# Performance work log

Hardware: AMD Instinct MI355X
Metric: run time of the kernel (lower is better)

## Reference

```python
import jax, jax.numpy as jnp
import numpy as np

TAU = 0.5
EPS = 1e-08
NORM_EPS = 1e-12  # F.normalize clamp

BS = 4096
D = 256


def _l2_normalize(x):
    n = jnp.linalg.norm(x, axis=1, keepdims=True)
    return x / jnp.maximum(n, NORM_EPS)


def setup_inputs() -> dict:
    key = jax.random.key(0)
    k1, k2 = jax.random.split(key)
    zi = jax.random.normal(k1, (BS, D), dtype=jnp.float32)
    zj = jax.random.normal(k2, (BS, D), dtype=jnp.float32)
    return {"zi": zi, "zj": zj}


def reference(zi, zj):
    bs = zi.shape[0]
    zi_n = _l2_normalize(zi)
    zj_n = _l2_normalize(zj)
    z = jnp.concatenate([zi_n, zj_n], axis=0)  # [2bs, d]
    # cosine sim of unit vectors == dot product
    sim = (z @ z.T) / TAU  # [2bs, 2bs]
    # positive pairs: (i, i+bs) and (i+bs, i) -> same diag values twice
    pos_diag = jnp.sum(zi_n * zj_n, axis=1) / TAU  # [bs]
    sim_pos = jnp.exp(jnp.concatenate([pos_diag, pos_diag]))  # [2bs]
    # negatives: all off-diagonal entries per row
    exp_sim = jnp.exp(sim)
    neg_sum = jnp.sum(exp_sim, axis=1) - jnp.diagonal(exp_sim)  # [2bs]
    loss = jnp.mean(-jnp.log(sim_pos / (neg_sum + EPS)))
    return loss
```

## Files before the change

kernel.cpp:

```cpp
#include <hip/hip_runtime.h>

#define N_TOT 8192
#define BSZ   4096
#define DIM   256

typedef __attribute__((ext_vector_type(4))) float f32x4;
typedef __attribute__((ext_vector_type(2))) unsigned long long u64x2;

#define PRESCALE 1.69864362f

__device__ __forceinline__ void async_copy16(const void* g, void* l) {
    __builtin_amdgcn_global_load_lds((const __attribute__((address_space(1))) void*)g,
                                     (__attribute__((address_space(3))) void*)l,
                                     16, 0, 0);
}

__global__ __launch_bounds__(256) void norm_kernel(const float* __restrict__ zi,
                                                   const float* __restrict__ zj,
                                                   unsigned char* __restrict__ zb,
                                                   float* __restrict__ posPart) {
    __shared__ float buf[2][256];
    const int wid  = threadIdx.x >> 6;
    const int lane = threadIdx.x & 63;
    const int pair = blockIdx.x * 2 + (wid & 1);
    const bool isZj = (wid >= 2);
    const float* src = isZj ? (zj + (size_t)pair * DIM) : (zi + (size_t)pair * DIM);
    float4 v = ((const float4*)src)[lane];
    float ss = v.x * v.x + v.y * v.y + v.z * v.z + v.w * v.w;
    #pragma unroll
    for (int off = 1; off < 64; off <<= 1) ss += __shfl_xor(ss, off);
    float inv = 1.0f / fmaxf(sqrtf(ss), 1e-12f);
    float4 nv = make_float4(v.x * inv, v.y * inv, v.z * inv, v.w * inv);

    const int outRow = isZj ? (pair + BSZ) : pair;
    const int j8  = lane >> 1;
    const int off4 = ((j8 >> 3) << 6) + ((j8 & 3) << 4) + (((j8 >> 2) & 1) << 3)
                   + ((lane & 1) << 2);
    int pk = __builtin_amdgcn_cvt_pk_fp8_f32(nv.x * PRESCALE, nv.y * PRESCALE, 0, false);
    pk     = __builtin_amdgcn_cvt_pk_fp8_f32(nv.z * PRESCALE, nv.w * PRESCALE, pk, true);
    *(int*)(zb + (size_t)outRow * 256 + off4) = pk;

    if (!isZj) ((float4*)&buf[wid & 1][0])[lane] = nv;
    __syncthreads();
    if (isZj) {
        float4 a = ((float4*)&buf[wid & 1][0])[lane];
        float d = a.x * nv.x + a.y * nv.y + a.z * nv.z + a.w * nv.w;
        #pragma unroll
        for (int off = 1; off < 64; off <<= 1) d += __shfl_xor(d, off);
        if (lane == 0) posPart[pair] = d;
    }
}

__global__ __launch_bounds__(256, 4) void sim_kernel(const unsigned char* __restrict__ zb,
                                                     float* __restrict__ partial) {
    __shared__ alignas(16) char smem[32768];

    const int t    = threadIdx.x;
    const int lane = t & 63;
    const int wid  = t >> 6;
    const int wr   = wid >> 1;
    const int wc   = wid & 1;
    const int g    = lane >> 4;
    const int c15  = lane & 15;

    const int k = blockIdx.x;
    int bi = (int)((129.0f - sqrtf(16641.0f - 8.0f * (float)k)) * 0.5f);
    while (bi * 64 - bi * (bi - 1) / 2 > k) bi--;
    while ((bi + 1) * 64 - (bi + 1) * bi / 2 <= k) bi++;
    const int bj = bi + (k - (bi * 64 - bi * (bi - 1) / 2));
    const bool diag = (bi == bj);

    const int row0 = bi * 128;
    const int col0 = bj * 128;

    f32x4 acc[4][4];
    #pragma unroll
    for (int m = 0; m < 4; m++)
        #pragma unroll
        for (int n = 0; n < 4; n++) acc[m][n] = (f32x4){0.f, 0.f, 0.f, 0.f};

    #define STAGE(b, kt) do {                                                   \
        _Pragma("unroll")                                                       \
        for (int i = 0; i < 2; i++) {                                           \
            const int e_  = i * 256 + t;                   \
            const int rr_ = e_ >> 2;                       \
            const int p_  = e_ & 3;                             \
            const int g_  = p_ ^ ((rr_ >> 1) & 3);           \
            char* lb = smem + (b) * 16384 + (i * 256 + wid * 64) * 16;          \
            async_copy16(zb + (size_t)(row0 + rr_) * 256 + (kt) * 64 + g_ * 16, \
                         lb);                                                   \
            async_copy16(zb + (size_t)(col0 + rr_) * 256 + (kt) * 64 + g_ * 16, \
                         lb + 8192);                                            \
        } } while (0)

    STAGE(0, 0);

    #pragma unroll
    for (int kt = 0; kt < 4; ++kt) {
        const int cur = kt & 1;
        if (kt < 3) {
            STAGE(cur ^ 1, kt + 1);
            asm volatile("s_waitcnt vmcnt(4)" ::: "memory");
        } else {
            asm volatile("s_waitcnt vmcnt(0)" ::: "memory");
        }
        __builtin_amdgcn_sched_barrier(0);
        __builtin_amdgcn_s_barrier();

        const char* Ab = smem + cur * 16384;
        const char* Bb = Ab + 8192;
        u64x2 af[4], bfr[4];
        #pragma unroll
        for (int m = 0; m < 4; m++) {
            const int rr = wr * 64 + m * 16 + c15;
            const int p  = g ^ ((rr >> 1) & 3);
            af[m] = *(const u64x2*)(Ab + rr * 64 + p * 16);
        }
        #pragma unroll
        for (int n = 0; n < 4; n++) {
            const int rr = wc * 64 + n * 16 + c15;
            const int p  = g ^ ((rr >> 1) & 3);
            bfr[n] = *(const u64x2*)(Bb + rr * 64 + p * 16);
        }
        #pragma unroll
        for (int m = 0; m < 4; m++)
            #pragma unroll
            for (int n = 0; n < 4; n++) {
                acc[m][n] = __builtin_amdgcn_mfma_f32_16x16x32_fp8_fp8(
                    (long)af[m].x, (long)bfr[n].x, acc[m][n], 0, 0, 0);
                acc[m][n] = __builtin_amdgcn_mfma_f32_16x16x32_fp8_fp8(
                    (long)af[m].y, (long)bfr[n].y, acc[m][n], 0, 0, 0);
            }

        __builtin_amdgcn_sched_barrier(0);
        __builtin_amdgcn_s_barrier();
    }
    #undef STAGE

    float rsum[4][4];
    float csum[4];
    #pragma unroll
    for (int m = 0; m < 4; m++)
        #pragma unroll
        for (int j = 0; j < 4; j++) rsum[m][j] = 0.f;
    #pragma unroll
    for (int n = 0; n < 4; n++) csum[n] = 0.f;

    const int colbase = col0 + wc * 64 + c15;
    const int rowbase = row0 + wr * 64 + (g << 2);
    #pragma unroll
    for (int m = 0; m < 4; m++) {
        #pragma unroll
        for (int n = 0; n < 4; n++) {
            const int colg = colbase + n * 16;
            #pragma unroll
            for (int j = 0; j < 4; j++) {
                const int rowg = rowbase + m * 16 + j;
                float e = exp2f(acc[m][n][j]);
                if (diag && rowg == colg) e = 0.0f;
                rsum[m][j] += e;
                csum[n] += e;
            }
        }
    }

    if (!diag) {
        #pragma unroll
        for (int n = 0; n < 4; n++) {
            float s = csum[n];
            s += __shfl_xor(s, 16);
            s += __shfl_xor(s, 32);
            csum[n] = s;
        }
        if (lane < 16) {
            float* dst = partial + (size_t)(bi * 2 + wr) * N_TOT;
            #pragma unroll
            for (int n = 0; n < 4; n++)
                dst[colbase + n * 16] = csum[n];
        }
    }

    float* sw = (float*)smem + wid * 1280;
    #pragma unroll
    for (int m = 0; m < 4; m++)
        #pragma unroll
        for (int j = 0; j < 4; j++)
            sw[(m * 16 + (g << 2) + j) * 20 + c15] = rsum[m][j];
    asm volatile("s_waitcnt lgkmcnt(0)" ::: "memory");
    __builtin_amdgcn_sched_barrier(0);
    f32x4 v0 = *(const f32x4*)(sw + lane * 20 + 0);
    f32x4 v1 = *(const f32x4*)(sw + lane * 20 + 4);
    f32x4 v2 = *(const f32x4*)(sw + lane * 20 + 8);
    f32x4 v3 = *(const f32x4*)(sw + lane * 20 + 12);
    float tot = (v0[0] + v0[1] + v0[2] + v0[3]) + (v1[0] + v1[1] + v1[2] + v1[3])
              + (v2[0] + v2[1] + v2[2] + v2[3]) + (v3[0] + v3[1] + v3[2] + v3[3]);
    partial[(size_t)(bj * 2 + wc) * N_TOT + row0 + wr * 64 + lane] = tot;
}

__global__ __launch_bounds__(256) void rowlog_kernel(const float* __restrict__ partial,
                                                     float* __restrict__ logPart) {
    const int lane = threadIdx.x & 63;
    const int w    = threadIdx.x >> 6;
    const int row  = blockIdx.x * 64 + lane;
    float s = 0.f;
    #pragma unroll 8
    for (int p = w * 32; p < w * 32 + 32; p++) s += partial[(size_t)p * N_TOT + row];
    __shared__ float red[4][64];
    red[w][lane] = s;
    __syncthreads();
    if (w == 0) {
        float tot = red[0][lane] + red[1][lane] + red[2][lane] + red[3][lane];
        float v = logf(tot + 1e-8f);
        #pragma unroll
        for (int off = 1; off < 64; off <<= 1) v += __shfl_xor(v, off);
        if (lane == 0) logPart[blockIdx.x] = v;
    }
}

__global__ __launch_bounds__(256) void final_kernel(const float* __restrict__ logPart,
                                                    const float* __restrict__ posPart,
                                                    float* __restrict__ out) {
    const int t = threadIdx.x;
    float ps = 0.f;
    for (int i = t; i < BSZ; i += 256) ps += posPart[i];
    float ls = (t < 128) ? logPart[t] : 0.f;
    #pragma unroll
    for (int off = 1; off < 64; off <<= 1) {
        ps += __shfl_xor(ps, off);
        ls += __shfl_xor(ls, off);
    }
    __shared__ float redp[4], redl[4];
    const int lane = t & 63, wid = t >> 6;
    if (lane == 0) { redp[wid] = ps; redl[wid] = ls; }
    __syncthreads();
    if (t == 0) {
        const float posSum = redp[0] + redp[1] + redp[2] + redp[3];
        const float logSum = redl[0] + redl[1] + redl[2] + redl[3];
        out[0] = logSum / (float)N_TOT - 2.0f * posSum / (float)BSZ;
    }
}

extern "C" void kernel_launch(void* const* d_in, const int* in_sizes, int n_in,
                              void* d_out, int out_size, void* d_ws, size_t ws_size,
                              hipStream_t stream) {
    const float* zi = (const float*)d_in[0];
    const float* zj = (const float*)d_in[1];
    float* out = (float*)d_out;

    char* ws = (char*)d_ws;
    unsigned char* zb = (unsigned char*)ws;
    float* partial     = (float*)(ws + (size_t)(4 << 20));
    float* logPart     = (float*)(ws + (size_t)(8 << 20));
    float* posPart     = (float*)(ws + (size_t)(8 << 20) + 4096);

    norm_kernel<<<2048, 256, 0, stream>>>(zi, zj, zb, posPart);
    sim_kernel<<<2080, 256, 0, stream>>>(zb, partial);
    rowlog_kernel<<<128, 256, 0, stream>>>(partial, logPart);
    final_kernel<<<1, 256, 0, stream>>>(logPart, posPart, out);
}
```

Before: 38.57 us.

## Switch sim GEMM to scaled 16x16x128 FP8 MFMA with two-stage full-K loads

Replaces the pairs of 16x16x32 fp8 MFMAs with the gfx950 scaled 16x16x128 f8f6f4 MFMA (unit scales), which cuts the instruction count per K-step. The fp8 row layout is changed to plain linear order and the LDS swizzle is redone for 128-byte K chunks. Both K halves are loaded into a doubled 64KB LDS buffer up front, replacing the 4-step double-buffered loop. Occupancy hint drops from 4 to 2 blocks per CU, which reduces latency hiding across blocks.

```diff
diff --git a/kernel.cpp b/kernel.cpp
--- a/kernel.cpp
+++ b/kernel.cpp
@@ -5,9 +5,11 @@
 #define DIM   256
 
 typedef __attribute__((ext_vector_type(4))) float f32x4;
-typedef __attribute__((ext_vector_type(2))) unsigned long long u64x2;
+typedef __attribute__((ext_vector_type(4))) int   i32x4;
+typedef __attribute__((ext_vector_type(8))) int   i32x8;
 
 #define PRESCALE 1.69864362f
+#define SCALE1   0x7F7F7F7F
 
 __device__ __forceinline__ void async_copy16(const void* g, void* l) {
     __builtin_amdgcn_global_load_lds((const __attribute__((address_space(1))) void*)g,
@@ -33,12 +35,9 @@
     float4 nv = make_float4(v.x * inv, v.y * inv, v.z * inv, v.w * inv);
 
     const int outRow = isZj ? (pair + BSZ) : pair;
-    const int j8  = lane >> 1;
-    const int off4 = ((j8 >> 3) << 6) + ((j8 & 3) << 4) + (((j8 >> 2) & 1) << 3)
-                   + ((lane & 1) << 2);
     int pk = __builtin_amdgcn_cvt_pk_fp8_f32(nv.x * PRESCALE, nv.y * PRESCALE, 0, false);
     pk     = __builtin_amdgcn_cvt_pk_fp8_f32(nv.z * PRESCALE, nv.w * PRESCALE, pk, true);
-    *(int*)(zb + (size_t)outRow * 256 + off4) = pk;
+    *(int*)(zb + (size_t)outRow * 256 + lane * 4) = pk;
 
     if (!isZj) ((float4*)&buf[wid & 1][0])[lane] = nv;
     __syncthreads();
@@ -51,9 +50,9 @@
     }
 }
 
-__global__ __launch_bounds__(256, 4) void sim_kernel(const unsigned char* __restrict__ zb,
+__global__ __launch_bounds__(256, 2) void sim_kernel(const unsigned char* __restrict__ zb,
                                                      float* __restrict__ partial) {
-    __shared__ alignas(16) char smem[32768];
+    __shared__ alignas(16) char smem[65536];
 
     const int t    = threadIdx.x;
     const int lane = t & 63;
@@ -79,63 +78,63 @@
         #pragma unroll
         for (int n = 0; n < 4; n++) acc[m][n] = (f32x4){0.f, 0.f, 0.f, 0.f};
 
-    #define STAGE(b, kt) do {                                                   \
+    #define STAGE(kt) do {                                                      \
         _Pragma("unroll")                                                       \
-        for (int i = 0; i < 2; i++) {                                           \
-            const int e_  = i * 256 + t;                   \
-            const int rr_ = e_ >> 2;                       \
-            const int p_  = e_ & 3;                             \
-            const int g_  = p_ ^ ((rr_ >> 1) & 3);           \
-            char* lb = smem + (b) * 16384 + (i * 256 + wid * 64) * 16;          \
-            async_copy16(zb + (size_t)(row0 + rr_) * 256 + (kt) * 64 + g_ * 16, \
-                         lb);                                                   \
-            async_copy16(zb + (size_t)(col0 + rr_) * 256 + (kt) * 64 + g_ * 16, \
-                         lb + 8192);                                            \
+        for (int i = 0; i < 4; i++) {                                           \
+            const int e_  = i * 256 + t;                  \
+            const int rr_ = e_ >> 3;                       \
+            const int c_  = (e_ & 7) ^ (((rr_ >> 2) & 1) << 1);                 \
+            char* lb = smem + (kt) * 32768 + (i * 256 + wid * 64) * 16;         \
+            const size_t ko = (size_t)(kt) * 128 + c_ * 16;                     \
+            async_copy16(zb + (size_t)(row0 + rr_) * 256 + ko, lb);             \
+            async_copy16(zb + (size_t)(col0 + rr_) * 256 + ko, lb + 16384);     \
         } } while (0)
 
-    STAGE(0, 0);
-
-    #pragma unroll
-    for (int kt = 0; kt < 4; ++kt) {
-        const int cur = kt & 1;
-        if (kt < 3) {
-            STAGE(cur ^ 1, kt + 1);
-            asm volatile("s_waitcnt vmcnt(4)" ::: "memory");
-        } else {
-            asm volatile("s_waitcnt vmcnt(0)" ::: "memory");
-        }
-        __builtin_amdgcn_sched_barrier(0);
-        __builtin_amdgcn_s_barrier();
-
-        const char* Ab = smem + cur * 16384;
-        const char* Bb = Ab + 8192;
-        u64x2 af[4], bfr[4];
+    STAGE(0);
+    STAGE(1);
+    asm volatile("s_waitcnt vmcnt(8)" ::: "memory");
+    __builtin_amdgcn_sched_barrier(0);
+    __builtin_amdgcn_s_barrier();
+
+    #pragma unroll
+    for (int kt = 0; kt < 2; ++kt) {
+        const char* Ab = smem + kt * 32768;
+        const char* Bb = Ab + 16384;
+        i32x8 af[4], bfr[4];
         #pragma unroll
         for (int m = 0; m < 4; m++) {
             const int rr = wr * 64 + m * 16 + c15;
-            const int p  = g ^ ((rr >> 1) & 3);
-            af[m] = *(const u64x2*)(Ab + rr * 64 + p * 16);
+            const int pp = g ^ ((rr >> 2) & 1);
+            i32x4 lo = *(const i32x4*)(Ab + rr * 128 + pp * 32);
+            i32x4 hi = *(const i32x4*)(Ab + rr * 128 + pp * 32 + 16);
+            af[m] = __builtin_shufflevector(lo, hi, 0, 1, 2, 3, 4, 5, 6, 7);
         }
         #pragma unroll
         for (int n = 0; n < 4; n++) {
             const int rr = wc * 64 + n * 16 + c15;
-            const int p  = g ^ ((rr >> 1) & 3);
-            bfr[n] = *(const u64x2*)(Bb + rr * 64 + p * 16);
+            const int pp = g ^ ((rr >> 2) & 1);
+            i32x4 lo = *(const i32x4*)(Bb + rr * 128 + pp * 32);
+            i32x4 hi = *(const i32x4*)(Bb + rr * 128 + pp * 32 + 16);
+            bfr[n] = __builtin_shufflevector(lo, hi, 0, 1, 2, 3, 4, 5, 6, 7);
         }
         #pragma unroll
         for (int m = 0; m < 4; m++)
             #pragma unroll
-            for (int n = 0; n < 4; n++) {
-                acc[m][n] = __builtin_amdgcn_mfma_f32_16x16x32_fp8_fp8(
-                    (long)af[m].x, (long)bfr[n].x, acc[m][n], 0, 0, 0);
-                acc[m][n] = __builtin_amdgcn_mfma_f32_16x16x32_fp8_fp8(
-                    (long)af[m].y, (long)bfr[n].y, acc[m][n], 0, 0, 0);
-            }
-
-        __builtin_amdgcn_sched_barrier(0);
-        __builtin_amdgcn_s_barrier();
+            for (int n = 0; n < 4; n++)
+                acc[m][n] = __builtin_amdgcn_mfma_scale_f32_16x16x128_f8f6f4(
+                    af[m], bfr[n], acc[m][n], 0, 0, 0, SCALE1, 0, SCALE1);
+
+        if (kt == 0) {
+            asm volatile("s_waitcnt vmcnt(0)" ::: "memory");
+            __builtin_amdgcn_sched_barrier(0);
+            __builtin_amdgcn_s_barrier();
+        }
     }
     #undef STAGE
+
+    asm volatile("s_waitcnt lgkmcnt(0)" ::: "memory");
+    __builtin_amdgcn_sched_barrier(0);
+    __builtin_amdgcn_s_barrier();
 
     float rsum[4][4];
     float csum[4];
```

Measured after the change: 41.41 us. +7.4%, slower.

## Switch similarity GEMM to 32x32x64 scaled FP8 MFMA with new LDS layout

Applied to the files above, without the earlier changes.

Replaces the 16x16x32 FP8 MFMA tiles with the 32x32x64 f8f6f4 scaled MFMA (unit scales), so each wave issues 4 large MFMAs per k-step instead of 32 small ones. The FP8 row layout in global memory is made contiguous, the LDS swizzle is changed to match the new fragment loads, and the epilogue row/column reductions are rewritten for the 32x32 accumulator layout with a swizzled LDS transpose. This cuts instruction issue and fragment-load overhead at the cost of a more complex epilogue and larger per-lane fragments.

```diff
diff --git a/kernel.cpp b/kernel.cpp
--- a/kernel.cpp
+++ b/kernel.cpp
@@ -4,10 +4,13 @@
 #define BSZ   4096
 #define DIM   256
 
-typedef __attribute__((ext_vector_type(4))) float f32x4;
-typedef __attribute__((ext_vector_type(2))) unsigned long long u64x2;
+typedef __attribute__((ext_vector_type(4)))  float f32x4;
+typedef __attribute__((ext_vector_type(16))) float f32x16;
+typedef __attribute__((ext_vector_type(4)))  int   i32x4;
+typedef __attribute__((ext_vector_type(8)))  int   i32x8;
 
 #define PRESCALE 1.69864362f
+#define SCALE1   0x7F7F7F7F
 
 __device__ __forceinline__ void async_copy16(const void* g, void* l) {
     __builtin_amdgcn_global_load_lds((const __attribute__((address_space(1))) void*)g,
@@ -33,12 +36,9 @@
     float4 nv = make_float4(v.x * inv, v.y * inv, v.z * inv, v.w * inv);
 
     const int outRow = isZj ? (pair + BSZ) : pair;
-    const int j8  = lane >> 1;
-    const int off4 = ((j8 >> 3) << 6) + ((j8 & 3) << 4) + (((j8 >> 2) & 1) << 3)
-                   + ((lane & 1) << 2);
     int pk = __builtin_amdgcn_cvt_pk_fp8_f32(nv.x * PRESCALE, nv.y * PRESCALE, 0, false);
     pk     = __builtin_amdgcn_cvt_pk_fp8_f32(nv.z * PRESCALE, nv.w * PRESCALE, pk, true);
-    *(int*)(zb + (size_t)outRow * 256 + off4) = pk;
+    *(int*)(zb + (size_t)outRow * 256 + lane * 4) = pk;
 
     if (!isZj) ((float4*)&buf[wid & 1][0])[lane] = nv;
     __syncthreads();
@@ -60,8 +60,8 @@
     const int wid  = t >> 6;
     const int wr   = wid >> 1;
     const int wc   = wid & 1;
-    const int g    = lane >> 4;
-    const int c15  = lane & 15;
+    const int hi   = lane >> 5;
+    const int r31  = lane & 31;
 
     const int k = blockIdx.x;
     int bi = (int)((129.0f - sqrtf(16641.0f - 8.0f * (float)k)) * 0.5f);
@@ -73,11 +73,13 @@
     const int row0 = bi * 128;
     const int col0 = bj * 128;
 
-    f32x4 acc[4][4];
-    #pragma unroll
-    for (int m = 0; m < 4; m++)
-        #pragma unroll
-        for (int n = 0; n < 4; n++) acc[m][n] = (f32x4){0.f, 0.f, 0.f, 0.f};
+    f32x16 acc[2][2];
+    #pragma unroll
+    for (int mt = 0; mt < 2; mt++)
+        #pragma unroll
+        for (int nt = 0; nt < 2; nt++)
+            #pragma unroll
+            for (int r = 0; r < 16; r++) acc[mt][nt][r] = 0.f;
 
     #define STAGE(b, kt) do {                                                   \
         _Pragma("unroll")                                                       \
@@ -85,7 +87,7 @@
             const int e_  = i * 256 + t;                   \
             const int rr_ = e_ >> 2;                       \
             const int p_  = e_ & 3;                             \
-            const int g_  = p_ ^ ((rr_ >> 1) & 3);           \
+            const int g_  = p_ ^ ((rr_ >> 2) & 3);           \
             char* lb = smem + (b) * 16384 + (i * 256 + wid * 64) * 16;          \
             async_copy16(zb + (size_t)(row0 + rr_) * 256 + (kt) * 64 + g_ * 16, \
                          lb);                                                   \
@@ -109,91 +111,72 @@
 
         const char* Ab = smem + cur * 16384;
         const char* Bb = Ab + 8192;
-        u64x2 af[4], bfr[4];
-        #pragma unroll
-        for (int m = 0; m < 4; m++) {
-            const int rr = wr * 64 + m * 16 + c15;
-            const int p  = g ^ ((rr >> 1) & 3);
-            af[m] = *(const u64x2*)(Ab + rr * 64 + p * 16);
-        }
-        #pragma unroll
-        for (int n = 0; n < 4; n++) {
-            const int rr = wc * 64 + n * 16 + c15;
-            const int p  = g ^ ((rr >> 1) & 3);
-            bfr[n] = *(const u64x2*)(Bb + rr * 64 + p * 16);
-        }
-        #pragma unroll
-        for (int m = 0; m < 4; m++)
+        i32x8 af[2], bfr[2];
+        #pragma unroll
+        for (int mt = 0; mt < 2; mt++) {
+            const int rr = wr * 64 + mt * 32 + r31;
+            const int s  = (rr >> 2) & 3;
+            i32x4 lo = *(const i32x4*)(Ab + rr * 64 + ((hi * 2)     ^ s) * 16);
+            i32x4 hv = *(const i32x4*)(Ab + rr * 64 + ((hi * 2 + 1) ^ s) * 16);
+            af[mt] = __builtin_shufflevector(lo, hv, 0, 1, 2, 3, 4, 5, 6, 7);
+        }
+        #pragma unroll
+        for (int nt = 0; nt < 2; nt++) {
+            const int rr = wc * 64 + nt * 32 + r31;
+            const int s  = (rr >> 2) & 3;
+            i32x4 lo = *(const i32x4*)(Bb + rr * 64 + ((hi * 2)     ^ s) * 16);
+            i32x4 hv = *(const i32x4*)(Bb + rr * 64 + ((hi * 2 + 1) ^ s) * 16);
+            bfr[nt] = __builtin_shufflevector(lo, hv, 0, 1, 2, 3, 4, 5, 6, 7);
+        }
+        #pragma unroll
+        for (int mt = 0; mt < 2; mt++)
             #pragma unroll
-            for (int n = 0; n < 4; n++) {
-                acc[m][n] = __builtin_amdgcn_mfma_f32_16x16x32_fp8_fp8(
-                    (long)af[m].x, (long)bfr[n].x, acc[m][n], 0, 0, 0);
-                acc[m][n] = __builtin_amdgcn_mfma_f32_16x16x32_fp8_fp8(
-                    (long)af[m].y, (long)bfr[n].y, acc[m][n], 0, 0, 0);
-            }
+            for (int nt = 0; nt < 2; nt++)
+                acc[mt][nt] = __builtin_amdgcn_mfma_scale_f32_32x32x64_f8f6f4(
+                    af[mt], bfr[nt], acc[mt][nt], 0, 0, 0, SCALE1, 0, SCALE1);
 
         __builtin_amdgcn_sched_barrier(0);
         __builtin_amdgcn_s_barrier();
     }
     #undef STAGE
 
-    float rsum[4][4];
-    float csum[4];
-    #pragma unroll
-    for (int m = 0; m < 4; m++)
-        #pragma unroll
-        for (int j = 0; j < 4; j++) rsum[m][j] = 0.f;
-    #pragma unroll
-    for (int n = 0; n < 4; n++) csum[n] = 0.f;
-
-    const int colbase = col0 + wc * 64 + c15;
-    const int rowbase = row0 + wr * 64 + (g << 2);
-    #pragma unroll
-    for (int m = 0; m < 4; m++) {
-        #pragma unroll
-        for (int n = 0; n < 4; n++) {
-            const int colg = colbase + n * 16;
+    float* sw = (float*)smem + wid * 2048;
+    float csum[2] = {0.f, 0.f};
+
+    #pragma unroll
+    for (int mt = 0; mt < 2; mt++) {
+        #pragma unroll
+        for (int reg = 0; reg < 16; reg++) {
+            const int row_l = mt * 32 + (reg & 3) + ((reg >> 2) << 3) + (hi << 2);
+            const int rowg  = row0 + wr * 64 + row_l;
+            float r = 0.f;
             #pragma unroll
-            for (int j = 0; j < 4; j++) {
-                const int rowg = rowbase + m * 16 + j;
-                float e = exp2f(acc[m][n][j]);
-                if (diag && rowg == colg) e = 0.0f;
-                rsum[m][j] += e;
-                csum[n] += e;
+            for (int nt = 0; nt < 2; nt++) {
+                float e = exp2f(acc[mt][nt][reg]);
+                if (diag && rowg == (col0 + wc * 64 + nt * 32 + r31)) e = 0.0f;
+                r += e;
+                csum[nt] += e;
             }
+            sw[row_l * 32 + ((((r31 >> 2) ^ (row_l & 7))) << 2) + (r31 & 3)] = r;
         }
     }
 
     if (!diag) {
-        #pragma unroll
-        for (int n = 0; n < 4; n++) {
-            float s = csum[n];
-            s += __shfl_xor(s, 16);
-            s += __shfl_xor(s, 32);
-            csum[n] = s;
-        }
-        if (lane < 16) {
-            float* dst = partial + (size_t)(bi * 2 + wr) * N_TOT;
-            #pragma unroll
-            for (int n = 0; n < 4; n++)
-                dst[colbase + n * 16] = csum[n];
-        }
-    }
-
-    float* sw = (float*)smem + wid * 1280;
-    #pragma unroll
-    for (int m = 0; m < 4; m++)
-        #pragma unroll
-        for (int j = 0; j < 4; j++)
-            sw[(m * 16 + (g << 2) + j) * 20 + c15] = rsum[m][j];
+        float cv0 = csum[0] + __shfl_xor(csum[0], 32);
+        float cv1 = csum[1] + __shfl_xor(csum[1], 32);
+        const float cv = hi ? cv1 : cv0;
+        partial[(size_t)(bi * 2 + wr) * N_TOT + col0 + wc * 64 + lane] = cv;
+    }
+
     asm volatile("s_waitcnt lgkmcnt(0)" ::: "memory");
     __builtin_amdgcn_sched_barrier(0);
-    f32x4 v0 = *(const f32x4*)(sw + lane * 20 + 0);
-    f32x4 v1 = *(const f32x4*)(sw + lane * 20 + 4);
-    f32x4 v2 = *(const f32x4*)(sw + lane * 20 + 8);
-    f32x4 v3 = *(const f32x4*)(sw + lane * 20 + 12);
-    float tot = (v0[0] + v0[1] + v0[2] + v0[3]) + (v1[0] + v1[1] + v1[2] + v1[3])
-              + (v2[0] + v2[1] + v2[2] + v2[3]) + (v3[0] + v3[1] + v3[2] + v3[3]);
+    float tot = 0.f;
+    #pragma unroll
+    for (int q = 0; q < 8; q++) {
+        const int ch = q ^ (lane & 7);
+        f32x4 v = *(const f32x4*)(sw + lane * 32 + ch * 4);
+        tot += v[0] + v[1] + v[2] + v[3];
+    }
     partial[(size_t)(bj * 2 + wc) * N_TOT + row0 + wr * 64 + lane] = tot;
 }
 
```

Result: no change. 38.63 us (median of 2 runs) (+0.2%).
